# Kernel tuning notes

Hardware: AMD Instinct MI355X
Metric: run time of the kernel (lower is better)

Reference implementation:

```python
import jax, jax.numpy as jnp
import numpy as np

IN_F, OUT_F = 4096, 14336
F8_MAX = 448.0  # max magnitude of float8_e4m3fn


def setup_inputs() -> dict:
    key = jax.random.key(0)
    kx, kw, kb = jax.random.split(key, 3)
    x = jax.random.normal(kx, (2, 512, IN_F), dtype=jnp.bfloat16)
    w = jax.random.normal(kw, (OUT_F, IN_F), dtype=jnp.float32) * 0.02
    # per-tensor scale: amax / 448 (as in F8Linear.__init__)
    w_scale = (jnp.maximum(jnp.abs(w).max(), 1e-30) / F8_MAX).astype(jnp.float32)
    # quantize to fp8 e4m3; roundtrip back to float32 so the stored values are
    # exactly the fp8-representable values (float32 container keeps the bwd
    # reference's jax.vjp happy while the math is identical)
    w_f8 = jnp.clip(w / w_scale, -F8_MAX, F8_MAX).astype(jnp.float8_e4m3fn).astype(jnp.float32)
    bias = jax.random.normal(kb, (OUT_F,), dtype=jnp.float32) * 0.02
    return {"x": x, "weight_f8": w_f8, "w_scale": w_scale, "bias": bias}


def reference(x, weight_f8, w_scale, bias):
    # dequantize to activation dtype, then GEMM: y = x @ w^T + b
    w = weight_f8.astype(x.dtype) * w_scale.astype(x.dtype)   # [out, in]
    y = jnp.einsum('bsi,oi->bso', x, w) + bias.astype(x.dtype)
    return y
```

## Files before the change

kernel.cpp:

```cpp
#include <hip/hip_runtime.h>
#include <hip/hip_bf16.h>
#include <stdint.h>


#define IN_F   4096
#define OUT_F  14336
#define M_TOT  1024

#define BM 128
#define BN 128

#define TM 256
#define TN 256
#define TK 64
#define KT8 (IN_F / TK)

typedef __bf16  bf16x8 __attribute__((ext_vector_type(8)));
typedef __bf16  bf16x4 __attribute__((ext_vector_type(4)));
typedef float   f32x4  __attribute__((ext_vector_type(4)));

__device__ __forceinline__ void async_copy16(const void* g, void* l) {
    __builtin_amdgcn_global_load_lds(
        (const __attribute__((address_space(1))) void*)g,
        (__attribute__((address_space(3))) void*)l,
        16, 0, 0);
}

__global__ void detect_x_dtype(const uint32_t* __restrict__ xb,
                               int* __restrict__ flag) {
    __shared__ int any_low;
    if (threadIdx.x == 0) any_low = 0;
    __syncthreads();
    uint32_t bad = 0;
    for (int i = threadIdx.x; i < 1024; i += 256) bad |= (xb[i] & 0xFFFFu);
    if (bad) atomicOr(&any_low, 1);
    __syncthreads();
    if (threadIdx.x == 0) *flag = (any_low == 0) ? 1 : 0;
}

__global__ __launch_bounds__(256) void cvt_w_kernel(
    const f32x4* __restrict__ in, bf16x8* __restrict__ out) {
    const int stride = 3584 * 256;
    for (int i = blockIdx.x * 256 + threadIdx.x; i < 7340032; i += stride) {
        f32x4 a = in[2 * i];
        f32x4 b = in[2 * i + 1];
        bf16x8 o;
        o[0] = (__bf16)a[0]; o[1] = (__bf16)a[1];
        o[2] = (__bf16)a[2]; o[3] = (__bf16)a[3];
        o[4] = (__bf16)b[0]; o[5] = (__bf16)b[1];
        o[6] = (__bf16)b[2]; o[7] = (__bf16)b[3];
        out[i] = o;
    }
}

__global__ __launch_bounds__(256) void cvt_x_kernel(
    const void* __restrict__ xraw, bf16x8* __restrict__ out,
    const int* __restrict__ flag) {
    const int f32w = (*flag != 0);
    const int i = blockIdx.x * 256 + threadIdx.x;
    if (f32w) {
        const f32x4* in = (const f32x4*)xraw;
        f32x4 a = in[2 * i];
        f32x4 b = in[2 * i + 1];
        bf16x8 o;
        o[0] = (__bf16)a[0]; o[1] = (__bf16)a[1];
        o[2] = (__bf16)a[2]; o[3] = (__bf16)a[3];
        o[4] = (__bf16)b[0]; o[5] = (__bf16)b[1];
        o[6] = (__bf16)b[2]; o[7] = (__bf16)b[3];
        out[i] = o;
    } else {
        out[i] = ((const bf16x8*)xraw)[i];
    }
}

__global__ __launch_bounds__(512, 2) void gemm_bf16_8ph(
    const __bf16* __restrict__ xb,
    const __bf16* __restrict__ wb,
    const float*  __restrict__ w_scale,
    const float*  __restrict__ bias,
    void*         __restrict__ yraw,
    const int*    __restrict__ flag_p)
{
    __shared__ __align__(16) __bf16 As[2][2][128 * TK];
    __shared__ __align__(16) __bf16 Bs[2][2][128 * TK];

    const int f32w = (*flag_p != 0);
    const int t    = threadIdx.x;
    const int lane = t & 63;
    const int wv   = t >> 6;
    const int wm   = wv >> 2;
    const int wn   = wv & 3;
    const int lidx = lane & 15;
    const int q    = lane >> 4;

    const int flat = blockIdx.x;
    const int xcd  = flat & 7;
    const int slot = flat >> 3;
    const int ni   = xcd * 7 + (slot >> 2);
    const int mi   = slot & 3;
    const int m0   = mi * TM;
    const int n0   = ni * TN;

    const float scale = w_scale[0];

    const __bf16* gA = xb + (size_t)m0 * IN_F;
    const __bf16* gB = wb + (size_t)n0 * IN_F;

    int srow[2], scgl[2];
    #pragma unroll
    for (int i = 0; i < 2; ++i) {
        const int s = i * 512 + t;
        srow[i] = s >> 3;
        scgl[i] = (s & 7) ^ (srow[i] & 7);
    }

    int aoff[4][2], boff[2][2];
    #pragma unroll
    for (int qm = 0; qm < 4; ++qm) {
        const int row = qm * 32 + wm * 16 + lidx;
        #pragma unroll
        for (int kg = 0; kg < 2; ++kg)
            aoff[qm][kg] = row * 128 + (((kg * 4 + q) ^ (row & 7)) * 16);
    }
    #pragma unroll
    for (int qn = 0; qn < 2; ++qn) {
        const int row = qn * 64 + wn * 16 + lidx;
        #pragma unroll
        for (int kg = 0; kg < 2; ++kg)
            boff[qn][kg] = row * 128 + (((kg * 4 + q) ^ (row & 7)) * 16);
    }

    const f32x4 zero4 = {0.f, 0.f, 0.f, 0.f};
    f32x4 acc[8][4];
    #pragma unroll
    for (int i = 0; i < 8; ++i)
        #pragma unroll
        for (int j = 0; j < 4; ++j)
            acc[i][j] = zero4;

    bf16x8 areg[4][2], breg[2][2];

#define STAGE_A(tile, half) do {                                              \
    __bf16* _dst = &As[(tile) & 1][(half)][0];                                \
    const __bf16* _src = gA + (size_t)(half) * 128 * IN_F + (tile) * TK;      \
    async_copy16(_src + (size_t)srow[0] * IN_F + scgl[0] * 8, _dst + t * 8);  \
    async_copy16(_src + (size_t)srow[1] * IN_F + scgl[1] * 8,                 \
                 _dst + (512 + t) * 8);                                       \
} while (0)

#define STAGE_B(tile, half) do {                                              \
    __bf16* _dst = &Bs[(tile) & 1][(half)][0];                                \
    const __bf16* _src = gB + (size_t)(half) * 128 * IN_F + (tile) * TK;      \
    async_copy16(_src + (size_t)srow[0] * IN_F + scgl[0] * 8, _dst + t * 8);  \
    async_copy16(_src + (size_t)srow[1] * IN_F + scgl[1] * 8,                 \
                 _dst + (512 + t) * 8);                                       \
} while (0)

#define LOAD_A(base) do {                                                     \
    _Pragma("unroll")                                                         \
    for (int _qm = 0; _qm < 4; ++_qm) {                                       \
        areg[_qm][0] = *(const bf16x8*)((base) + aoff[_qm][0]);               \
        areg[_qm][1] = *(const bf16x8*)((base) + aoff[_qm][1]);               \
    }                                                                         \
} while (0)

#define LOAD_B(base) do {                                                     \
    _Pragma("unroll")                                                         \
    for (int _qn = 0; _qn < 2; ++_qn) {                                       \
        breg[_qn][0] = *(const bf16x8*)((base) + boff[_qn][0]);               \
        breg[_qn][1] = *(const bf16x8*)((base) + boff[_qn][1]);               \
    }                                                                         \
} while (0)

#define MFMA16(MO, NO) do {                                                   \
    __builtin_amdgcn_s_setprio(1);                                            \
    _Pragma("unroll")                                                         \
    for (int _qm = 0; _qm < 4; ++_qm)                                         \
        _Pragma("unroll")                                                     \
        for (int _qn = 0; _qn < 2; ++_qn) {                                   \
            acc[(MO) + _qm][(NO) + _qn] =                                     \
                __builtin_amdgcn_mfma_f32_16x16x32_bf16(                      \
                    areg[_qm][0], breg[_qn][0], acc[(MO) + _qm][(NO) + _qn],  \
                    0, 0, 0);                                                 \
            acc[(MO) + _qm][(NO) + _qn] =                                     \
                __builtin_amdgcn_mfma_f32_16x16x32_bf16(                      \
                    areg[_qm][1], breg[_qn][1], acc[(MO) + _qm][(NO) + _qn],  \
                    0, 0, 0);                                                 \
        }                                                                     \
    __builtin_amdgcn_s_setprio(0);                                            \
} while (0)

#define BARR() __builtin_amdgcn_s_barrier()
#define LGKM0() do {                                                          \
    asm volatile("s_waitcnt lgkmcnt(0)" ::: "memory");                        \
    __builtin_amdgcn_sched_barrier(0);                                        \
} while (0)

    STAGE_A(0, 0); STAGE_B(0, 1); STAGE_B(0, 0); STAGE_A(0, 1);
    STAGE_A(1, 0); STAGE_B(1, 1);
    asm volatile("s_waitcnt vmcnt(4)" ::: "memory");
    BARR();

    for (int kt = 0; kt < KT8; ++kt) {
        const char* a0 = (const char*)&As[kt & 1][0][0];
        const char* a1 = (const char*)&As[kt & 1][1][0];
        const char* b0 = (const char*)&Bs[kt & 1][0][0];
        const char* b1 = (const char*)&Bs[kt & 1][1][0];

        LOAD_A(a0);
        LOAD_B(b0);
        if (kt + 1 < KT8) STAGE_B(kt + 1, 0);
        BARR(); LGKM0();
        MFMA16(0, 0);
        BARR();

        LOAD_B(b1);
        if (kt + 1 < KT8) STAGE_A(kt + 1, 1);
        BARR(); LGKM0();
        MFMA16(0, 2);
        BARR();

        LOAD_A(a1);
        if (kt + 2 < KT8) STAGE_A(kt + 2, 0);
        BARR(); LGKM0();
        MFMA16(4, 2);
        BARR();

        LOAD_B(b0);
        if (kt + 2 < KT8) STAGE_B(kt + 2, 1);
        BARR(); LGKM0();
        MFMA16(4, 0);
        if (kt < KT8 - 2) asm volatile("s_waitcnt vmcnt(4)" ::: "memory");
        else              asm volatile("s_waitcnt vmcnt(0)" ::: "memory");
        BARR();
    }

#undef STAGE_A
#undef STAGE_B
#undef LOAD_A
#undef LOAD_B
#undef MFMA16
#undef BARR
#undef LGKM0

    float bv[4];
    #pragma unroll
    for (int nf = 0; nf < 4; ++nf)
        bv[nf] = bias[n0 + (nf >> 1) * 128 + (nf & 1) * 64 + wn * 16 + lidx];

    if (f32w) {
        float* yf = (float*)yraw;
        #pragma unroll
        for (int mf = 0; mf < 8; ++mf)
            #pragma unroll
            for (int r = 0; r < 4; ++r) {
                const int m = m0 + (mf >> 2) * 128 + (mf & 3) * 32 + wm * 16 + q * 4 + r;
                float* yp = yf + (size_t)m * OUT_F + n0 + wn * 16 + lidx;
                #pragma unroll
                for (int nf = 0; nf < 4; ++nf)
                    yp[(nf >> 1) * 128 + (nf & 1) * 64] =
                        acc[mf][nf][r] * scale + bv[nf];
            }
    } else {
        __bf16* yh = (__bf16*)yraw;
        #pragma unroll
        for (int mf = 0; mf < 8; ++mf)
            #pragma unroll
            for (int r = 0; r < 4; ++r) {
                const int m = m0 + (mf >> 2) * 128 + (mf & 3) * 32 + wm * 16 + q * 4 + r;
                __bf16* yp = yh + (size_t)m * OUT_F + n0 + wn * 16 + lidx;
                #pragma unroll
                for (int nf = 0; nf < 4; ++nf)
                    yp[(nf >> 1) * 128 + (nf & 1) * 64] =
                        (__bf16)(acc[mf][nf][r] * scale + bv[nf]);
            }
    }
}

__global__ __launch_bounds__(256) void f8linear_fallback(
    const void*  __restrict__ xraw,
    const float* __restrict__ wq,
    const float* __restrict__ w_scale,
    const float* __restrict__ bias,
    void*        __restrict__ yraw,
    const int*   __restrict__ flag_p)
{
    __shared__ __align__(16) __bf16 As[BM * 40];
    __shared__ __align__(16) __bf16 Bs[BN * 40];

    const int f32w = (*flag_p != 0);
    const int t    = threadIdx.x;
    const int lane = t & 63;
    const int wv   = t >> 6;
    const int wm   = wv >> 1;
    const int wn   = wv & 1;
    const int lidx = lane & 15;
    const int q    = lane >> 4;

    const int flat = blockIdx.x;
    const int xcd  = flat & 7;
    const int slot = flat >> 3;
    const int ni   = xcd * 14 + (slot >> 3);
    const int mi   = slot & 7;
    const int m0   = mi * BM;
    const int n0   = ni * BN;

    const float scale = w_scale[0];
    const float*  xf = (const float*)xraw;
    const __bf16* xh = (const __bf16*)xraw;

    const int af_row = t >> 3;
    const int af_col = (t & 7) * 4;
    int ah_row[2], ah_cg[2];
    #pragma unroll
    for (int i = 0; i < 2; ++i) {
        const int s = i * 256 + t;
        ah_row[i] = s >> 2;
        ah_cg[i]  = s & 3;
    }
    const int b_row = t >> 3;
    const int b_col = (t & 7) * 4;

    const f32x4 zero4 = {0.f, 0.f, 0.f, 0.f};
    f32x4 acc[4][4];
    #pragma unroll
    for (int i = 0; i < 4; ++i)
        #pragma unroll
        for (int j = 0; j < 4; ++j)
            acc[i][j] = zero4;

    f32x4  aregf[4];
    bf16x8 aregh[2];
    f32x4  breg[4];
    if (f32w) {
        #pragma unroll
        for (int i = 0; i < 4; ++i)
            aregf[i] = *reinterpret_cast<const f32x4*>(
                xf + (size_t)(m0 + af_row + i * 32) * IN_F + af_col);
    } else {
        #pragma unroll
        for (int i = 0; i < 2; ++i)
            aregh[i] = *reinterpret_cast<const bf16x8*>(
                xh + (size_t)(m0 + ah_row[i]) * IN_F + ah_cg[i] * 8);
    }
    #pragma unroll
    for (int i = 0; i < 4; ++i)
        breg[i] = *reinterpret_cast<const f32x4*>(
            wq + (size_t)(n0 + i * 32 + b_row) * IN_F + b_col);

    for (int kt = 0; kt < 128; ++kt) {
        const int k0 = kt * 32;
        if (f32w) {
            #pragma unroll
            for (int i = 0; i < 4; ++i) {
                bf16x4 pk;
                pk[0] = (__bf16)aregf[i][0];
                pk[1] = (__bf16)aregf[i][1];
                pk[2] = (__bf16)aregf[i][2];
                pk[3] = (__bf16)aregf[i][3];
                *reinterpret_cast<bf16x4*>(As + (af_row + i * 32) * 40 + af_col) = pk;
            }
        } else {
            #pragma unroll
            for (int i = 0; i < 2; ++i)
                *reinterpret_cast<bf16x8*>(As + ah_row[i] * 40 + ah_cg[i] * 8) = aregh[i];
        }
        #pragma unroll
        for (int i = 0; i < 4; ++i) {
            bf16x4 pk;
            pk[0] = (__bf16)breg[i][0];
            pk[1] = (__bf16)breg[i][1];
            pk[2] = (__bf16)breg[i][2];
            pk[3] = (__bf16)breg[i][3];
            *reinterpret_cast<bf16x4*>(Bs + (i * 32 + b_row) * 40 + b_col) = pk;
        }
        __syncthreads();
        if (kt + 1 < 128) {
            const int k1 = k0 + 32;
            if (f32w) {
                #pragma unroll
                for (int i = 0; i < 4; ++i)
                    aregf[i] = *reinterpret_cast<const f32x4*>(
                        xf + (size_t)(m0 + af_row + i * 32) * IN_F + k1 + af_col);
            } else {
                #pragma unroll
                for (int i = 0; i < 2; ++i)
                    aregh[i] = *reinterpret_cast<const bf16x8*>(
                        xh + (size_t)(m0 + ah_row[i]) * IN_F + k1 + ah_cg[i] * 8);
            }
            #pragma unroll
            for (int i = 0; i < 4; ++i)
                breg[i] = *reinterpret_cast<const f32x4*>(
                    wq + (size_t)(n0 + i * 32 + b_row) * IN_F + k1 + b_col);
        }
        bf16x8 afr[4], bfr[4];
        #pragma unroll
        for (int mt = 0; mt < 4; ++mt) {
            const int row = wm * 64 + mt * 16 + lidx;
            afr[mt] = *reinterpret_cast<const bf16x8*>(As + row * 40 + q * 8);
        }
        #pragma unroll
        for (int nt = 0; nt < 4; ++nt) {
            const int row = wn * 64 + nt * 16 + lidx;
            bfr[nt] = *reinterpret_cast<const bf16x8*>(Bs + row * 40 + q * 8);
        }
        #pragma unroll
        for (int mt = 0; mt < 4; ++mt)
            #pragma unroll
            for (int nt = 0; nt < 4; ++nt)
                acc[mt][nt] = __builtin_amdgcn_mfma_f32_16x16x32_bf16(
                    afr[mt], bfr[nt], acc[mt][nt], 0, 0, 0);
        __syncthreads();
    }

    float bv[4];
    #pragma unroll
    for (int nt = 0; nt < 4; ++nt)
        bv[nt] = bias[n0 + wn * 64 + nt * 16 + lidx];

    if (f32w) {
        float* yf = (float*)yraw;
        #pragma unroll
        for (int mt = 0; mt < 4; ++mt)
            #pragma unroll
            for (int r = 0; r < 4; ++r) {
                const int m = m0 + wm * 64 + mt * 16 + q * 4 + r;
                float* yp = yf + (size_t)m * OUT_F + n0 + wn * 64 + lidx;
                #pragma unroll
                for (int nt = 0; nt < 4; ++nt)
                    yp[nt * 16] = acc[mt][nt][r] * scale + bv[nt];
            }
    } else {
        __bf16* yh = (__bf16*)yraw;
        #pragma unroll
        for (int mt = 0; mt < 4; ++mt)
            #pragma unroll
            for (int r = 0; r < 4; ++r) {
                const int m = m0 + wm * 64 + mt * 16 + q * 4 + r;
                __bf16* yp = yh + (size_t)m * OUT_F + n0 + wn * 64 + lidx;
                #pragma unroll
                for (int nt = 0; nt < 4; ++nt)
                    yp[nt * 16] = (__bf16)(acc[mt][nt][r] * scale + bv[nt]);
            }
    }
}

extern "C" void kernel_launch(void* const* d_in, const int* in_sizes, int n_in,
                              void* d_out, int out_size, void* d_ws, size_t ws_size,
                              hipStream_t stream) {
    const void* px = nullptr; const void* pw = nullptr;
    const void* ps = nullptr; const void* pb = nullptr;
    for (int i = 0; i < n_in; ++i) {
        const long sz = in_sizes[i];
        if      (sz == (long)M_TOT * IN_F) px = d_in[i];
        else if (sz == (long)OUT_F * IN_F) pw = d_in[i];
        else if (sz == 1)                  ps = d_in[i];
        else if (sz == OUT_F)              pb = d_in[i];
    }
    if (!px) px = d_in[0];
    if (!pw) pw = d_in[1];
    if (!ps) ps = d_in[2];
    if (!pb) pb = d_in[3];

    const size_t W_BYTES  = (size_t)OUT_F * IN_F * 2;
    const size_t X_OFF    = W_BYTES;
    const size_t X_BYTES  = (size_t)M_TOT * IN_F * 2;
    const size_t FLAG_OFF = X_OFF + X_BYTES;

    if (ws_size >= FLAG_OFF + 16) {
        __bf16* wbf  = (__bf16*)d_ws;
        __bf16* xbf  = (__bf16*)((char*)d_ws + X_OFF);
        int*    flag = (int*)((char*)d_ws + FLAG_OFF);

        const int grid8 = (M_TOT / TM) * (OUT_F / TN);

        detect_x_dtype<<<1, 256, 0, stream>>>((const uint32_t*)px, flag);
        cvt_w_kernel<<<3584, 256, 0, stream>>>((const f32x4*)pw, (bf16x8*)wbf);
        cvt_x_kernel<<<2048, 256, 0, stream>>>(px, (bf16x8*)xbf, flag);
        gemm_bf16_8ph<<<grid8, 512, 0, stream>>>(
            xbf, wbf, (const float*)ps, (const float*)pb, d_out, flag);
    } else {
        int* flag = (int*)d_ws;
        const int grid = (M_TOT / BM) * (OUT_F / BN);
        detect_x_dtype<<<1, 256, 0, stream>>>((const uint32_t*)px, flag);
        f8linear_fallback<<<grid, 256, 0, stream>>>(
            px, (const float*)pw, (const float*)ps, (const float*)pb, d_out, flag);
    }
}
```

Measured before the change: 528.3 us.

## Fuse fp32 weight conversion into GEMM B-tile loading via registers

Removes the separate weight fp32-to-bf16 conversion kernel and its workspace buffer. The GEMM now loads fp32 weight tiles straight into registers, converts them to bf16 and writes them to LDS. This replaces async global-to-LDS copies for B, with vmcnt waits rescheduled around the new loads. It saves a full pass that read 235MB and wrote 117MB, but the GEMM now reads fp32 weights (twice the bytes per tile, re-read by 4 M-blocks) and uses more registers for staging.

```diff
diff --git a/kernel.cpp b/kernel.cpp
--- a/kernel.cpp
+++ b/kernel.cpp
@@ -36,21 +36,6 @@
     if (bad) atomicOr(&any_low, 1);
     __syncthreads();
     if (threadIdx.x == 0) *flag = (any_low == 0) ? 1 : 0;
-}
-
-__global__ __launch_bounds__(256) void cvt_w_kernel(
-    const f32x4* __restrict__ in, bf16x8* __restrict__ out) {
-    const int stride = 3584 * 256;
-    for (int i = blockIdx.x * 256 + threadIdx.x; i < 7340032; i += stride) {
-        f32x4 a = in[2 * i];
-        f32x4 b = in[2 * i + 1];
-        bf16x8 o;
-        o[0] = (__bf16)a[0]; o[1] = (__bf16)a[1];
-        o[2] = (__bf16)a[2]; o[3] = (__bf16)a[3];
-        o[4] = (__bf16)b[0]; o[5] = (__bf16)b[1];
-        o[6] = (__bf16)b[2]; o[7] = (__bf16)b[3];
-        out[i] = o;
-    }
 }
 
 __global__ __launch_bounds__(256) void cvt_x_kernel(
@@ -73,9 +58,9 @@
     }
 }
 
-__global__ __launch_bounds__(512, 2) void gemm_bf16_8ph(
+__global__ __launch_bounds__(512, 2) void gemm_fused_8ph(
     const __bf16* __restrict__ xb,
-    const __bf16* __restrict__ wb,
+    const float*  __restrict__ wf,
     const float*  __restrict__ w_scale,
     const float*  __restrict__ bias,
     void*         __restrict__ yraw,
@@ -104,7 +89,6 @@
     const float scale = w_scale[0];
 
     const __bf16* gA = xb + (size_t)m0 * IN_F;
-    const __bf16* gB = wb + (size_t)n0 * IN_F;
 
     int srow[2], scgl[2];
     #pragma unroll
@@ -114,6 +98,9 @@
         scgl[i] = (s & 7) ^ (srow[i] & 7);
     }
 
+    const float* gB0 = wf + (size_t)(n0 + srow[0]) * IN_F + scgl[0] * 8;
+    const float* gB1 = wf + (size_t)(n0 + srow[1]) * IN_F + scgl[1] * 8;
+
     int aoff[4][2], boff[2][2];
     #pragma unroll
     for (int qm = 0; qm < 4; ++qm) {
@@ -139,6 +126,7 @@
             acc[i][j] = zero4;
 
     bf16x8 areg[4][2], breg[2][2];
+    f32x4  Br0[4], Br1[4];
 
 #define STAGE_A(tile, half) do {                                              \
     __bf16* _dst = &As[(tile) & 1][(half)][0];                                \
@@ -148,12 +136,28 @@
                  _dst + (512 + t) * 8);                                       \
 } while (0)
 
-#define STAGE_B(tile, half) do {                                              \
-    __bf16* _dst = &Bs[(tile) & 1][(half)][0];                                \
-    const __bf16* _src = gB + (size_t)(half) * 128 * IN_F + (tile) * TK;      \
-    async_copy16(_src + (size_t)srow[0] * IN_F + scgl[0] * 8, _dst + t * 8);  \
-    async_copy16(_src + (size_t)srow[1] * IN_F + scgl[1] * 8,                 \
-                 _dst + (512 + t) * 8);                                       \
+#define B_LOAD(tile, half, Rv) do {                                           \
+    const float* _p0 = gB0 + (size_t)(half) * 128 * IN_F + (tile) * TK;       \
+    const float* _p1 = gB1 + (size_t)(half) * 128 * IN_F + (tile) * TK;       \
+    Rv[0] = *(const f32x4*)_p0;                                               \
+    Rv[1] = *(const f32x4*)(_p0 + 4);                                         \
+    Rv[2] = *(const f32x4*)_p1;                                               \
+    Rv[3] = *(const f32x4*)(_p1 + 4);                                         \
+} while (0)
+
+#define B_WRITE(tile, half, Rv) do {                                          \
+    __bf16* _d = &Bs[(tile) & 1][(half)][0];                                  \
+    bf16x8 _o;                                                                \
+    _o[0] = (__bf16)Rv[0][0]; _o[1] = (__bf16)Rv[0][1];                       \
+    _o[2] = (__bf16)Rv[0][2]; _o[3] = (__bf16)Rv[0][3];                       \
+    _o[4] = (__bf16)Rv[1][0]; _o[5] = (__bf16)Rv[1][1];                       \
+    _o[6] = (__bf16)Rv[1][2]; _o[7] = (__bf16)Rv[1][3];                       \
+    *(bf16x8*)(_d + (size_t)t * 8) = _o;                                      \
+    _o[0] = (__bf16)Rv[2][0]; _o[1] = (__bf16)Rv[2][1];                       \
+    _o[2] = (__bf16)Rv[2][2]; _o[3] = (__bf16)Rv[2][3];                       \
+    _o[4] = (__bf16)Rv[3][0]; _o[5] = (__bf16)Rv[3][1];                       \
+    _o[6] = (__bf16)Rv[3][2]; _o[7] = (__bf16)Rv[3][3];                       \
+    *(bf16x8*)(_d + (size_t)(512 + t) * 8) = _o;                              \
 } while (0)
 
 #define LOAD_A(base) do {                                                     \
@@ -195,10 +199,18 @@
     asm volatile("s_waitcnt lgkmcnt(0)" ::: "memory");                        \
     __builtin_amdgcn_sched_barrier(0);                                        \
 } while (0)
-
-    STAGE_A(0, 0); STAGE_B(0, 1); STAGE_B(0, 0); STAGE_A(0, 1);
-    STAGE_A(1, 0); STAGE_B(1, 1);
-    asm volatile("s_waitcnt vmcnt(4)" ::: "memory");
+#define VMCNT(n) asm volatile("s_waitcnt vmcnt(" #n ")" ::: "memory")
+
+    B_LOAD(0, 0, Br0);
+    B_LOAD(0, 1, Br1);
+    STAGE_A(0, 0);
+    STAGE_A(0, 1);
+    STAGE_A(1, 0);
+    VMCNT(6);
+    B_WRITE(0, 0, Br0);
+    B_WRITE(0, 1, Br1);
+    VMCNT(2);
+    LGKM0();
     BARR();
 
     for (int kt = 0; kt < KT8; ++kt) {
@@ -209,39 +221,52 @@
 
         LOAD_A(a0);
         LOAD_B(b0);
-        if (kt + 1 < KT8) STAGE_B(kt + 1, 0);
+        if (kt + 1 < KT8) B_LOAD(kt + 1, 0, Br0);
         BARR(); LGKM0();
         MFMA16(0, 0);
         BARR();
 
         LOAD_B(b1);
-        if (kt + 1 < KT8) STAGE_A(kt + 1, 1);
+        if (kt + 1 < KT8) {
+            B_LOAD(kt + 1, 1, Br1);
+            STAGE_A(kt + 1, 1);
+        }
         BARR(); LGKM0();
         MFMA16(0, 2);
         BARR();
 
         LOAD_A(a1);
+        if (kt + 1 < KT8) {
+            VMCNT(6);
+            B_WRITE(kt + 1, 0, Br0);
+        }
         if (kt + 2 < KT8) STAGE_A(kt + 2, 0);
         BARR(); LGKM0();
         MFMA16(4, 2);
         BARR();
 
         LOAD_B(b0);
-        if (kt + 2 < KT8) STAGE_B(kt + 2, 1);
+        if (kt + 1 < KT8) {
+            if (kt + 2 < KT8) { VMCNT(4); } else { VMCNT(2); }
+            B_WRITE(kt + 1, 1, Br1);
+        }
         BARR(); LGKM0();
         MFMA16(4, 0);
-        if (kt < KT8 - 2) asm volatile("s_waitcnt vmcnt(4)" ::: "memory");
-        else              asm volatile("s_waitcnt vmcnt(0)" ::: "memory");
+        if (kt + 1 < KT8) {
+            if (kt + 2 < KT8) { VMCNT(2); } else { VMCNT(0); }
+        }
         BARR();
     }
 
 #undef STAGE_A
-#undef STAGE_B
+#undef B_LOAD
+#undef B_WRITE
 #undef LOAD_A
 #undef LOAD_B
 #undef MFMA16
 #undef BARR
 #undef LGKM0
+#undef VMCNT
 
     float bv[4];
     #pragma unroll
@@ -462,23 +487,20 @@
     if (!ps) ps = d_in[2];
     if (!pb) pb = d_in[3];
 
-    const size_t W_BYTES  = (size_t)OUT_F * IN_F * 2;
-    const size_t X_OFF    = W_BYTES;
     const size_t X_BYTES  = (size_t)M_TOT * IN_F * 2;
-    const size_t FLAG_OFF = X_OFF + X_BYTES;
+    const size_t FLAG_OFF = X_BYTES;
 
     if (ws_size >= FLAG_OFF + 16) {
-        __bf16* wbf  = (__bf16*)d_ws;
-        __bf16* xbf  = (__bf16*)((char*)d_ws + X_OFF);
+        __bf16* xbf  = (__bf16*)d_ws;
         int*    flag = (int*)((char*)d_ws + FLAG_OFF);
 
         const int grid8 = (M_TOT / TM) * (OUT_F / TN);
 
         detect_x_dtype<<<1, 256, 0, stream>>>((const uint32_t*)px, flag);
-        cvt_w_kernel<<<3584, 256, 0, stream>>>((const f32x4*)pw, (bf16x8*)wbf);
         cvt_x_kernel<<<2048, 256, 0, stream>>>(px, (bf16x8*)xbf, flag);
-        gemm_bf16_8ph<<<grid8, 512, 0, stream>>>(
-            xbf, wbf, (const float*)ps, (const float*)pb, d_out, flag);
+        gemm_fused_8ph<<<grid8, 512, 0, stream>>>(
+            xbf, (const float*)pw, (const float*)ps, (const float*)pb,
+            d_out, flag);
     } else {
         int* flag = (int*)d_ws;
         const int grid = (M_TOT / BM) * (OUT_F / BN);
```

After: 506.4 us. 4.1% less time.
